# Performance work log

Measured on AMD Instinct MI355X. Metric: run time of the kernel, lower is better.

The kernel has to match this reference:

```python
import jax, jax.numpy as jnp
import numpy as np

MAX_CH = 21
LAT_DIM = 64
D_EMBED = 1024
N_HEADS = 16
D_HEAD = D_EMBED // N_HEADS  # 64
L = MAX_CH * LAT_DIM         # 1344 latents
B, T = 4, 1024


def setup_inputs() -> dict:
    key = jax.random.key(0)
    k1, k2, k3, k4, k5, k6 = jax.random.split(key, 6)
    x = jax.random.normal(k1, (B, T, D_EMBED), dtype=jnp.float32)
    # boolean channel mask [b, L, T]
    ch_mask = jax.random.randint(k2, (B, L, T), 0, 2) > 0
    # learned latent queries [L, H*d] (xavier-uniform-ish init)
    lim_q = float(np.sqrt(6.0 / (L + N_HEADS * D_HEAD)))
    latent_q = jax.random.uniform(k3, (L, N_HEADS * D_HEAD), minval=-lim_q, maxval=lim_q, dtype=jnp.float32)
    # Linear weights (torch layout: [out, in]) and biases
    lim_w = float(np.sqrt(1.0 / D_EMBED))
    w_k_w = jax.random.uniform(k4, (N_HEADS * D_HEAD, D_EMBED), minval=-lim_w, maxval=lim_w, dtype=jnp.float32)
    w_k_b = jnp.zeros((N_HEADS * D_HEAD,), dtype=jnp.float32)
    w_v_w = jax.random.uniform(k5, (N_HEADS * D_HEAD, D_EMBED), minval=-lim_w, maxval=lim_w, dtype=jnp.float32)
    w_v_b = jax.random.uniform(k6, (N_HEADS * D_HEAD,), minval=-lim_w, maxval=lim_w, dtype=jnp.float32)
    return {"x": x, "ch_mask": ch_mask, "latent_q": latent_q,
            "w_k_w": w_k_w, "w_k_b": w_k_b, "w_v_w": w_v_w, "w_v_b": w_v_b}


def reference(x, ch_mask, latent_q, w_k_w, w_k_b, w_v_w, w_v_b):
    b, t, d = x.shape
    H, dh = N_HEADS, D_HEAD
    l = latent_q.shape[0]
    # faithful to torch .view(-1, H, L, d): raw row-major reinterpretation
    lq = latent_q.reshape(1, H, l, dh)                    # [1,H,L,dh]
    k = (x @ w_k_w.T + w_k_b).reshape(b, t, H, dh).transpose(0, 2, 3, 1)  # [b,H,dh,T]
    v = (x @ w_v_w.T + w_v_b).reshape(b, t, H, dh).transpose(0, 2, 1, 3)  # [b,H,T,dh]
    scale = jnp.float32(H) ** -0.5  # note: n_heads**-0.5, as in source
    scores = jnp.einsum('ohld,bhdt->bhlt', lq, k) * scale  # [b,H,L,T]
    mask = ch_mask[:, None, :, :]                           # [b,1,L,T] broadcast over heads
    scores = jnp.where(mask, scores, jnp.float32(-1e9))
    w = jax.nn.softmax(scores, axis=-1)
    w = jnp.where(mask, w, jnp.float32(0.0))
    out = jnp.einsum('bhlt,bhtd->bhld', w, v)               # [b,H,L,dh]
    return out.transpose(0, 2, 1, 3).reshape(b, l, H * dh)  # [b,L,H*dh]
```

## Files before the change

kernel.cpp:

```cpp
#include <hip/hip_runtime.h>
#include <hip/hip_bf16.h>

#define B_SZ 4
#define T_SZ 1024
#define NH 16
#define L_SZ 1344
#define LT_COUNT 21

typedef __attribute__((ext_vector_type(8))) short short8;
typedef __attribute__((ext_vector_type(4))) short short4v;
typedef __attribute__((ext_vector_type(4))) float floatx4;

typedef __attribute__((address_space(1))) const void gvoid;
typedef __attribute__((address_space(3))) void svoid;
#define GLD16(gp, lp) \
  __builtin_amdgcn_global_load_lds((gvoid*)(gp), (svoid*)(lp), 16, 0, 0)

static __device__ inline short bf16bits(float f) {
  return __builtin_bit_cast(short, __float2bfloat16(f));
}
static __device__ inline short4v cvt4(float4 v) {
  short4v r;
  r.x = bf16bits(v.x); r.y = bf16bits(v.y);
  r.z = bf16bits(v.z); r.w = bf16bits(v.w);
  return r;
}

static __device__ inline unsigned pack_bf16_2(float a, float b) {
  unsigned ua = __builtin_bit_cast(unsigned, a) + 0x8000u;
  unsigned ub = __builtin_bit_cast(unsigned, b) + 0x8000u;
  return __builtin_amdgcn_perm(ub, ua, 0x07060302u);
}
static __device__ inline uint2 pack_bf16_4(float4 v) {
  return make_uint2(pack_bf16_2(v.x, v.y), pack_bf16_2(v.z, v.w));
}


__global__ __launch_bounds__(256) void prep_kernel(
    const float4* __restrict__ x, const float4* __restrict__ wk,
    const float4* __restrict__ wv,
    uint2* __restrict__ xb, uint2* __restrict__ wkb, uint2* __restrict__ wvb,
    const void* __restrict__ mask, unsigned int* __restrict__ bits) {
  const int lane = threadIdx.x & 63;
  int f = -1;
  for (int vb = blockIdx.x; vb < 27648; vb += gridDim.x) {
    if (vb < 6144) {
      size_t i = (size_t)vb * 256 + threadIdx.x;
      if (i < 1048576)      xb[i] = pack_bf16_4(x[i]);
      else if (i < 1310720) wkb[i - 1048576] = pack_bf16_4(wk[i - 1048576]);
      else                  wvb[i - 1310720] = pack_bf16_4(wv[i - 1310720]);
    } else {
      if (f < 0) {
        const uint4* mp = (const uint4*)mask;
        uint4 a = mp[lane * 4 + 0], b2 = mp[lane * 4 + 1];
        uint4 c = mp[lane * 4 + 2], d = mp[lane * 4 + 3];
        unsigned oo = (a.x | a.y | a.z | a.w | b2.x | b2.y | b2.z | b2.w |
                       c.x | c.y | c.z | c.w | d.x | d.y | d.z | d.w) & 0xFFFFFF00u;
        unsigned aa = (a.y | a.w | b2.y | b2.w | c.y | c.w | d.y | d.w) & 0xFFu;
        int anyo = __any(oo != 0), anya = __any(aa != 0);
        f = anyo ? 1 : (anya ? 0 : 2);
      }
      int idx = (vb - 6144) * 256 + threadIdx.x;
      bool v;
      if (f == 1)      v = ((const signed char*)mask)[idx] != 0;
      else if (f == 2) v = ((const long long*)mask)[idx] != 0;
      else             v = ((const int*)mask)[idx] != 0;
      unsigned long long bal = __ballot(v);
      if ((lane & 31) == 0) {
        unsigned int w = (lane & 32) ? (unsigned int)(bal >> 32) : (unsigned int)bal;
        bits[idx >> 5] = w;
      }
    }
  }
}

__global__ __launch_bounds__(256, 4) void gemm_kv_bf16(
    const __hip_bfloat16* __restrict__ xb,
    const __hip_bfloat16* __restrict__ wkb, const __hip_bfloat16* __restrict__ wvb,
    const float* __restrict__ bk, const float* __restrict__ bv,
    __hip_bfloat16* __restrict__ k_buf, __hip_bfloat16* __restrict__ v_buf) {
  __shared__ __align__(16) __hip_bfloat16 ldsA[2][128 * 32];
  __shared__ __align__(16) __hip_bfloat16 ldsB[2][64 * 32];
  const int tid = threadIdx.x;
  const int lane = tid & 63, w = tid >> 6;
  const int wm = w & 1, wn = w >> 1;
  const int c15 = lane & 15, kq = lane >> 4;

  const __hip_bfloat16* A;
  const __hip_bfloat16* B;
  int TA, TB;
  if (blockIdx.z == 0) {
    A = wkb; B = xb; TA = blockIdx.x >> 6; TB = blockIdx.x & 63;
  } else {
    A = xb; B = wvb; TA = blockIdx.x >> 4; TB = blockIdx.x & 15;
  }
  const __hip_bfloat16* Abase = A + (size_t)TA * 128 * 1024;
  const __hip_bfloat16* Bbase = B + (size_t)TB * 64 * 1024;

  floatx4 acc[4][2];
  #pragma unroll
  for (int i = 0; i < 4; ++i)
    #pragma unroll
    for (int j = 0; j < 2; ++j) acc[i][j] = (floatx4){0.f, 0.f, 0.f, 0.f};

#define GSTAGE(sb, kk) do {                                                  \
    int cA_ = w * 128 + lane;                                                \
    int rA_ = cA_ >> 2, gA_ = (cA_ & 3) ^ (rA_ & 3);                         \
    GLD16(Abase + (size_t)rA_ * 1024 + (kk) + gA_ * 8,                       \
          &ldsA[sb][(w * 128) * 8]);                                         \
    int cA2_ = cA_ + 64;                                                     \
    int rA2_ = cA2_ >> 2, gA2_ = (cA2_ & 3) ^ (rA2_ & 3);                    \
    GLD16(Abase + (size_t)rA2_ * 1024 + (kk) + gA2_ * 8,                     \
          &ldsA[sb][(w * 128 + 64) * 8]);                                    \
    int cB_ = w * 64 + lane;                                                 \
    int rB_ = cB_ >> 2, gB_ = (cB_ & 3) ^ (rB_ & 3);                         \
    GLD16(Bbase + (size_t)rB_ * 1024 + (kk) + gB_ * 8,                       \
          &ldsB[sb][(w * 64) * 8]);                                          \
  } while (0)

  GSTAGE(0, 0);
  for (int kk = 0; kk < 1024; kk += 32) {
    const int buf = (kk >> 5) & 1;
    if (kk + 32 < 1024) {
      GSTAGE(buf ^ 1, kk + 32);
      asm volatile("s_waitcnt vmcnt(3)" ::: "memory");
    } else {
      asm volatile("s_waitcnt vmcnt(0)" ::: "memory");
    }
    __builtin_amdgcn_s_barrier();

    short8 af[4], bfr[2];
    #pragma unroll
    for (int mi = 0; mi < 4; ++mi) {
      int row = wm * 64 + mi * 16 + c15;
      af[mi] = *(const short8*)(&ldsA[buf][row * 32 + ((kq ^ (row & 3)) * 8)]);
    }
    #pragma unroll
    for (int ni = 0; ni < 2; ++ni) {
      int row = wn * 32 + ni * 16 + c15;
      bfr[ni] = *(const short8*)(&ldsB[buf][row * 32 + ((kq ^ (row & 3)) * 8)]);
    }
    #pragma unroll
    for (int mi = 0; mi < 4; ++mi)
      #pragma unroll
      for (int ni = 0; ni < 2; ++ni)
        acc[mi][ni] = __builtin_amdgcn_mfma_f32_16x16x32_bf16(
            af[mi], bfr[ni], acc[mi][ni], 0, 0, 0);

    asm volatile("s_waitcnt lgkmcnt(0)" ::: "memory");
    __builtin_amdgcn_s_barrier();
  }
#undef GSTAGE

  if (blockIdx.z == 0) {
    #pragma unroll
    for (int ni = 0; ni < 2; ++ni) {
      int gr = TB * 64 + wn * 32 + ni * 16 + c15;
      int b = gr >> 10, tc = (gr >> 6) & 15;
      int ni2 = (gr & 63) >> 4;
      #pragma unroll
      for (int mi = 0; mi < 4; ++mi) {
        int d0 = TA * 128 + wm * 64 + mi * 16 + kq * 4;
        int h = d0 >> 6, hd = d0 & 63;
        int half = hd >> 5, q4 = (hd >> 3) & 3, jlo = hd & 7;
        int bh = b * 16 + h;
        float4 b4 = *(const float4*)(bk + d0);
        float4 v4 = {acc[mi][ni][0] + b4.x, acc[mi][ni][1] + b4.y,
                     acc[mi][ni][2] + b4.z, acc[mi][ni][3] + b4.w};
        *(uint2*)(k_buf + ((size_t)((bh * 16 + tc) * 8 + ni2 * 2 + half)) * 512 +
                  (q4 * 16 + c15) * 8 + jlo) = pack_bf16_4(v4);
      }
    }
  } else {
    #pragma unroll
    for (int ni = 0; ni < 2; ++ni) {
      int d = TB * 64 + wn * 32 + ni * 16 + c15;
      int h = d >> 6;
      int di = (d & 63) >> 4;
      float bias = bv[d];
      #pragma unroll
      for (int mi = 0; mi < 4; ++mi) {
        int gr = TA * 128 + wm * 64 + mi * 16 + kq * 4;
        int b = gr >> 10, tc = (gr >> 6) & 15;
        int tl = gr & 63;
        int half = tl >> 5, q4 = (tl >> 3) & 3, jlo = tl & 7;
        int bh = b * 16 + h;
        float4 v4 = {acc[mi][ni][0] + bias, acc[mi][ni][1] + bias,
                     acc[mi][ni][2] + bias, acc[mi][ni][3] + bias};
        *(uint2*)(v_buf + ((size_t)((bh * 16 + tc) * 8 + di * 2 + half)) * 512 +
                  (q4 * 16 + c15) * 8 + jlo) = pack_bf16_4(v4);
      }
    }
  }
}

__global__ __launch_bounds__(256, 4) void attn_kernel(
    const float* __restrict__ latent_q,
    const __hip_bfloat16* __restrict__ k_buf,
    const __hip_bfloat16* __restrict__ v_buf,
    const unsigned int* __restrict__ mbits,
    float* __restrict__ out) {
  __shared__ __align__(16) __hip_bfloat16 ldsK[2][4096];
  __shared__ __align__(16) __hip_bfloat16 ldsV[2][4096];
  __shared__ __align__(16) __hip_bfloat16 pbuf[4][1024];

  const int tid = threadIdx.x;
  const int lane = tid & 63;
  const int w = tid >> 6;
  int bid = blockIdx.x;
  int xcd = bid & 7, j = bid >> 3;
  int bh = xcd * 8 + j / LT_COUNT;
  int lt = j % LT_COUNT;
  int h = bh & 15, b = bh >> 4;
  const int q4 = lane >> 4, c15 = lane & 15;
  const int c7 = c15 & 7;
  const int l0 = lt * 64;

  const float QS = 0.25f * 1.44269504089f;
  short8 qf[2];
  {
    const float* qp = latent_q + ((size_t)(h * L_SZ + l0 + w * 16 + c15)) * 64 + q4 * 8;
    float4 a0 = *(const float4*)(qp);
    float4 a1 = *(const float4*)(qp + 4);
    float4 a2 = *(const float4*)(qp + 32);
    float4 a3 = *(const float4*)(qp + 36);
    a0.x *= QS; a0.y *= QS; a0.z *= QS; a0.w *= QS;
    a1.x *= QS; a1.y *= QS; a1.z *= QS; a1.w *= QS;
    a2.x *= QS; a2.y *= QS; a2.z *= QS; a2.w *= QS;
    a3.x *= QS; a3.y *= QS; a3.z *= QS; a3.w *= QS;
    short4v t0 = cvt4(a0), t1 = cvt4(a1), t2 = cvt4(a2), t3 = cvt4(a3);
    qf[0] = (short8){t0.x, t0.y, t0.z, t0.w, t1.x, t1.y, t1.z, t1.w};
    qf[1] = (short8){t2.x, t2.y, t2.z, t2.w, t3.x, t3.y, t3.z, t3.w};
  }

  const short ob16 = (short)0x3F80;
  const short8 ones8 = (short8){ob16, ob16, ob16, ob16, ob16, ob16, ob16, ob16};
  const floatx4 zero4 = (floatx4){0.f, 0.f, 0.f, 0.f};

  floatx4 lacc = zero4;
  floatx4 o_acc[4];
  #pragma unroll
  for (int di = 0; di < 4; ++di) o_acc[di] = zero4;

  const __hip_bfloat16* kb = k_buf + (size_t)bh * 65536;
  const __hip_bfloat16* vb = v_buf + (size_t)bh * 65536;
  __hip_bfloat16* pw = pbuf[w];
  const unsigned int* mrow = mbits + ((size_t)(b * L_SZ + l0 + w * 16 + c15)) * 32;

#define STAGE_K(sb, tcn) do {                                               \
    const __hip_bfloat16* gk_ = kb + (size_t)(tcn) * 4096;                  \
    int o0_ = w * 512 + lane * 8;                                           \
    GLD16(gk_ + o0_,        &ldsK[sb][w * 512]);                            \
    GLD16(gk_ + 2048 + o0_, &ldsK[sb][2048 + w * 512]);                     \
  } while (0)
#define STAGE_V(sb, tcn) do {                                               \
    const __hip_bfloat16* gv_ = vb + (size_t)(tcn) * 4096;                  \
    int o0_ = w * 512 + lane * 8;                                           \
    GLD16(gv_ + o0_,        &ldsV[sb][w * 512]);                            \
    GLD16(gv_ + 2048 + o0_, &ldsV[sb][2048 + w * 512]);                     \
  } while (0)

  uint2 mw_cur = *(const uint2*)(mrow);
  STAGE_K(0, 0);
  STAGE_V(0, 0);

  for (int tc = 0; tc < 16; ++tc) {
    const int buf = tc & 1;
    if (tc < 15) {
      STAGE_K(buf ^ 1, tc + 1);
      asm volatile("s_waitcnt vmcnt(5)" ::: "memory");
    } else {
      asm volatile("s_waitcnt vmcnt(3)" ::: "memory");
    }
    __builtin_amdgcn_s_barrier();

    uint2 mw_nxt = mw_cur;
    if (tc < 15) mw_nxt = *(const uint2*)(mrow + (tc + 1) * 2);

    short8 kf[2][4];
    #pragma unroll
    for (int half = 0; half < 2; ++half)
      #pragma unroll
      for (int ni = 0; ni < 4; ++ni)
        kf[half][ni] = *(const short8*)(&ldsK[buf][(ni * 2 + half) * 512 + lane * 8]);
    floatx4 s[4];
    __builtin_amdgcn_s_setprio(1);
    #pragma unroll
    for (int ni = 0; ni < 4; ++ni)
      s[ni] = __builtin_amdgcn_mfma_f32_16x16x32_bf16(kf[0][ni], qf[0], zero4, 0, 0, 0);
    #pragma unroll
    for (int ni = 0; ni < 4; ++ni)
      s[ni] = __builtin_amdgcn_mfma_f32_16x16x32_bf16(kf[1][ni], qf[1], s[ni], 0, 0, 0);
    __builtin_amdgcn_s_setprio(0);

    if (tc < 15) {
      STAGE_V(buf ^ 1, tc + 1);
      asm volatile("s_waitcnt vmcnt(5)" ::: "memory");
    } else {
      asm volatile("s_waitcnt vmcnt(0)" ::: "memory");
    }
    __builtin_amdgcn_s_barrier();

    short8 vf[2][4];
    #pragma unroll
    for (int half = 0; half < 2; ++half)
      #pragma unroll
      for (int di = 0; di < 4; ++di)
        vf[half][di] = *(const short8*)(&ldsV[buf][(di * 2 + half) * 512 + lane * 8]);

    #pragma unroll
    for (int ni = 0; ni < 4; ++ni) {
      unsigned mword = (ni >= 2) ? mw_cur.y : mw_cur.x;
      float4 p4;
      #pragma unroll
      for (int r = 0; r < 4; ++r) {
        float e = exp2f(s[ni][r]);
        int sh = (ni & 1) * 16 + q4 * 4 + r;
        ((float*)&p4)[r] = ((mword >> sh) & 1) ? e : 0.f;
      }
      int pc = (ni * 2 + (q4 >> 1)) ^ c7;
      *(uint2*)(pw + c15 * 64 + pc * 8 + (q4 & 1) * 4) = pack_bf16_4(p4);
    }

    int pc0 = q4 ^ c7;
    short8 pf0 = *(const short8*)(pw + c15 * 64 + pc0 * 8);
    short8 pf1 = *(const short8*)(pw + c15 * 64 + (pc0 ^ 4) * 8);
    __builtin_amdgcn_s_setprio(1);
    #pragma unroll
    for (int di = 0; di < 4; ++di)
      o_acc[di] = __builtin_amdgcn_mfma_f32_16x16x32_bf16(vf[0][di], pf0, o_acc[di], 0, 0, 0);
    #pragma unroll
    for (int di = 0; di < 4; ++di)
      o_acc[di] = __builtin_amdgcn_mfma_f32_16x16x32_bf16(vf[1][di], pf1, o_acc[di], 0, 0, 0);
    lacc = __builtin_amdgcn_mfma_f32_16x16x32_bf16(ones8, pf0, lacc, 0, 0, 0);
    lacc = __builtin_amdgcn_mfma_f32_16x16x32_bf16(ones8, pf1, lacc, 0, 0, 0);
    __builtin_amdgcn_s_setprio(0);

    mw_cur = mw_nxt;
  }
#undef STAGE_K
#undef STAGE_V

  float la = lacc[0];
  float inv = (la > 0.f) ? 1.f / la : 0.f;
  float* ob = out + ((size_t)(b * L_SZ + l0 + w * 16 + c15)) * 1024 + h * 64;
  #pragma unroll
  for (int di = 0; di < 4; ++di) {
    float4 o4 = {o_acc[di][0] * inv, o_acc[di][1] * inv,
                 o_acc[di][2] * inv, o_acc[di][3] * inv};
    *(float4*)(ob + di * 16 + q4 * 4) = o4;
  }
}

extern "C" void kernel_launch(void* const* d_in, const int* in_sizes, int n_in,
                              void* d_out, int out_size, void* d_ws, size_t ws_size,
                              hipStream_t stream) {
  const float* x      = (const float*)d_in[0];
  const void* ch_mask = d_in[1];
  const float* lq     = (const float*)d_in[2];
  const float* wk     = (const float*)d_in[3];
  const float* bk     = (const float*)d_in[4];
  const float* wv     = (const float*)d_in[5];
  const float* bv     = (const float*)d_in[6];
  float* out = (float*)d_out;

  char* ws = (char*)d_ws;
  unsigned int* mbits   = (unsigned int*)ws;
  __hip_bfloat16* k_buf = (__hip_bfloat16*)(ws + 786432);
  __hip_bfloat16* v_buf = (__hip_bfloat16*)(ws + 786432 + 8388608);

  __hip_bfloat16* xb  = (__hip_bfloat16*)d_out;
  __hip_bfloat16* wkb = xb + 4 * 1024 * 1024;
  __hip_bfloat16* wvb = wkb + 1024 * 1024;

  prep_kernel<<<2048, 256, 0, stream>>>(
      (const float4*)x, (const float4*)wk, (const float4*)wv,
      (uint2*)xb, (uint2*)wkb, (uint2*)wvb,
      ch_mask, mbits);
  gemm_kv_bf16<<<dim3(512, 1, 2), 256, 0, stream>>>(xb, wkb, wvb, bk, bv, k_buf, v_buf);

  attn_kernel<<<8 * 168, 256, 0, stream>>>(lq, k_buf, v_buf, mbits, out);
}
```

Before: 189.2 us.

## Widen attention blocks to 8 waves covering 128 latents per K/V stage

The attention kernel now launches 512-thread blocks that each cover 128 latent rows, so each staged K/V tile is shared by 8 waves instead of 4. Each wave issues one async global-to-LDS load per tile instead of two, which halves the K/V traffic per latent. The cost is a ragged final block: 1344 is not a multiple of 128, so idle waves are guarded by a `has` flag but still join every barrier. Larger blocks may also lower occupancy and lengthen barrier stalls.

```diff
diff --git a/kernel.cpp b/kernel.cpp
--- a/kernel.cpp
+++ b/kernel.cpp
@@ -194,7 +194,7 @@
   }
 }
 
-__global__ __launch_bounds__(256, 4) void attn_kernel(
+__global__ __launch_bounds__(512, 6) void attn_kernel(
     const float* __restrict__ latent_q,
     const __hip_bfloat16* __restrict__ k_buf,
     const __hip_bfloat16* __restrict__ v_buf,
@@ -202,24 +202,27 @@
     float* __restrict__ out) {
   __shared__ __align__(16) __hip_bfloat16 ldsK[2][4096];
   __shared__ __align__(16) __hip_bfloat16 ldsV[2][4096];
-  __shared__ __align__(16) __hip_bfloat16 pbuf[4][1024];
+  __shared__ __align__(16) __hip_bfloat16 pbuf[8][1024];
 
   const int tid = threadIdx.x;
   const int lane = tid & 63;
   const int w = tid >> 6;
   int bid = blockIdx.x;
   int xcd = bid & 7, j = bid >> 3;
-  int bh = xcd * 8 + j / LT_COUNT;
-  int lt = j % LT_COUNT;
+  int bh = xcd * 8 + j / 11;
+  int sb = j % 11;
   int h = bh & 15, b = bh >> 4;
   const int q4 = lane >> 4, c15 = lane & 15;
   const int c7 = c15 & 7;
-  const int l0 = lt * 64;
+  const int l0 = sb * 128;
+  const int lg = l0 + w * 16;
+  const bool has = lg < L_SZ;
+  const int lrow = has ? lg : 0;
 
   const float QS = 0.25f * 1.44269504089f;
   short8 qf[2];
   {
-    const float* qp = latent_q + ((size_t)(h * L_SZ + l0 + w * 16 + c15)) * 64 + q4 * 8;
+    const float* qp = latent_q + ((size_t)(h * L_SZ + lrow + c15)) * 64 + q4 * 8;
     float4 a0 = *(const float4*)(qp);
     float4 a1 = *(const float4*)(qp + 4);
     float4 a2 = *(const float4*)(qp + 32);
@@ -245,110 +248,108 @@
   const __hip_bfloat16* kb = k_buf + (size_t)bh * 65536;
   const __hip_bfloat16* vb = v_buf + (size_t)bh * 65536;
   __hip_bfloat16* pw = pbuf[w];
-  const unsigned int* mrow = mbits + ((size_t)(b * L_SZ + l0 + w * 16 + c15)) * 32;
-
-#define STAGE_K(sb, tcn) do {                                               \
-    const __hip_bfloat16* gk_ = kb + (size_t)(tcn) * 4096;                  \
-    int o0_ = w * 512 + lane * 8;                                           \
-    GLD16(gk_ + o0_,        &ldsK[sb][w * 512]);                            \
-    GLD16(gk_ + 2048 + o0_, &ldsK[sb][2048 + w * 512]);                     \
-  } while (0)
-#define STAGE_V(sb, tcn) do {                                               \
-    const __hip_bfloat16* gv_ = vb + (size_t)(tcn) * 4096;                  \
-    int o0_ = w * 512 + lane * 8;                                           \
-    GLD16(gv_ + o0_,        &ldsV[sb][w * 512]);                            \
-    GLD16(gv_ + 2048 + o0_, &ldsV[sb][2048 + w * 512]);                     \
-  } while (0)
-
-  uint2 mw_cur = *(const uint2*)(mrow);
+  const unsigned int* mrow = mbits + ((size_t)(b * L_SZ + lrow + c15)) * 32;
+
+#define STAGE_K(sbuf, tcn) \
+    GLD16(kb + (size_t)(tcn) * 4096 + w * 512 + lane * 8, &ldsK[sbuf][w * 512])
+#define STAGE_V(sbuf, tcn) \
+    GLD16(vb + (size_t)(tcn) * 4096 + w * 512 + lane * 8, &ldsV[sbuf][w * 512])
+
   STAGE_K(0, 0);
   STAGE_V(0, 0);
+  uint2 mw_cur = *(const uint2*)(mrow);
 
   for (int tc = 0; tc < 16; ++tc) {
     const int buf = tc & 1;
     if (tc < 15) {
       STAGE_K(buf ^ 1, tc + 1);
-      asm volatile("s_waitcnt vmcnt(5)" ::: "memory");
+      asm volatile("s_waitcnt vmcnt(3)" ::: "memory");
     } else {
-      asm volatile("s_waitcnt vmcnt(3)" ::: "memory");
+      asm volatile("s_waitcnt vmcnt(2)" ::: "memory");
     }
     __builtin_amdgcn_s_barrier();
 
     uint2 mw_nxt = mw_cur;
     if (tc < 15) mw_nxt = *(const uint2*)(mrow + (tc + 1) * 2);
 
-    short8 kf[2][4];
-    #pragma unroll
-    for (int half = 0; half < 2; ++half)
+    floatx4 s[4];
+    if (has) {
+      short8 kf[2][4];
+      #pragma unroll
+      for (int half = 0; half < 2; ++half)
+        #pragma unroll
+        for (int ni = 0; ni < 4; ++ni)
+          kf[half][ni] = *(const short8*)(&ldsK[buf][(ni * 2 + half) * 512 + lane * 8]);
+      __builtin_amdgcn_s_setprio(1);
       #pragma unroll
       for (int ni = 0; ni < 4; ++ni)
-        kf[half][ni] = *(const short8*)(&ldsK[buf][(ni * 2 + half) * 512 + lane * 8]);
-    floatx4 s[4];
-    __builtin_amdgcn_s_setprio(1);
-    #pragma unroll
-    for (int ni = 0; ni < 4; ++ni)
-      s[ni] = __builtin_amdgcn_mfma_f32_16x16x32_bf16(kf[0][ni], qf[0], zero4, 0, 0, 0);
-    #pragma unroll
-    for (int ni = 0; ni < 4; ++ni)
-      s[ni] = __builtin_amdgcn_mfma_f32_16x16x32_bf16(kf[1][ni], qf[1], s[ni], 0, 0, 0);
-    __builtin_amdgcn_s_setprio(0);
+        s[ni] = __builtin_amdgcn_mfma_f32_16x16x32_bf16(kf[0][ni], qf[0], zero4, 0, 0, 0);
+      #pragma unroll
+      for (int ni = 0; ni < 4; ++ni)
+        s[ni] = __builtin_amdgcn_mfma_f32_16x16x32_bf16(kf[1][ni], qf[1], s[ni], 0, 0, 0);
+      __builtin_amdgcn_s_setprio(0);
+    }
 
     if (tc < 15) {
       STAGE_V(buf ^ 1, tc + 1);
-      asm volatile("s_waitcnt vmcnt(5)" ::: "memory");
+      asm volatile("s_waitcnt vmcnt(3)" ::: "memory");
     } else {
       asm volatile("s_waitcnt vmcnt(0)" ::: "memory");
     }
     __builtin_amdgcn_s_barrier();
 
-    short8 vf[2][4];
-    #pragma unroll
-    for (int half = 0; half < 2; ++half)
+    if (has) {
+      short8 vf[2][4];
+      #pragma unroll
+      for (int half = 0; half < 2; ++half)
+        #pragma unroll
+        for (int di = 0; di < 4; ++di)
+          vf[half][di] = *(const short8*)(&ldsV[buf][(di * 2 + half) * 512 + lane * 8]);
+
+      #pragma unroll
+      for (int ni = 0; ni < 4; ++ni) {
+        unsigned mword = (ni >= 2) ? mw_cur.y : mw_cur.x;
+        float4 p4;
+        #pragma unroll
+        for (int r = 0; r < 4; ++r) {
+          float e = exp2f(s[ni][r]);
+          int sh = (ni & 1) * 16 + q4 * 4 + r;
+          ((float*)&p4)[r] = ((mword >> sh) & 1) ? e : 0.f;
+        }
+        int pc = (ni * 2 + (q4 >> 1)) ^ c7;
+        *(uint2*)(pw + c15 * 64 + pc * 8 + (q4 & 1) * 4) = pack_bf16_4(p4);
+      }
+
+      int pc0 = q4 ^ c7;
+      short8 pf0 = *(const short8*)(pw + c15 * 64 + pc0 * 8);
+      short8 pf1 = *(const short8*)(pw + c15 * 64 + (pc0 ^ 4) * 8);
+      __builtin_amdgcn_s_setprio(1);
       #pragma unroll
       for (int di = 0; di < 4; ++di)
-        vf[half][di] = *(const short8*)(&ldsV[buf][(di * 2 + half) * 512 + lane * 8]);
-
-    #pragma unroll
-    for (int ni = 0; ni < 4; ++ni) {
-      unsigned mword = (ni >= 2) ? mw_cur.y : mw_cur.x;
-      float4 p4;
-      #pragma unroll
-      for (int r = 0; r < 4; ++r) {
-        float e = exp2f(s[ni][r]);
-        int sh = (ni & 1) * 16 + q4 * 4 + r;
-        ((float*)&p4)[r] = ((mword >> sh) & 1) ? e : 0.f;
-      }
-      int pc = (ni * 2 + (q4 >> 1)) ^ c7;
-      *(uint2*)(pw + c15 * 64 + pc * 8 + (q4 & 1) * 4) = pack_bf16_4(p4);
-    }
-
-    int pc0 = q4 ^ c7;
-    short8 pf0 = *(const short8*)(pw + c15 * 64 + pc0 * 8);
-    short8 pf1 = *(const short8*)(pw + c15 * 64 + (pc0 ^ 4) * 8);
-    __builtin_amdgcn_s_setprio(1);
-    #pragma unroll
-    for (int di = 0; di < 4; ++di)
-      o_acc[di] = __builtin_amdgcn_mfma_f32_16x16x32_bf16(vf[0][di], pf0, o_acc[di], 0, 0, 0);
-    #pragma unroll
-    for (int di = 0; di < 4; ++di)
-      o_acc[di] = __builtin_amdgcn_mfma_f32_16x16x32_bf16(vf[1][di], pf1, o_acc[di], 0, 0, 0);
-    lacc = __builtin_amdgcn_mfma_f32_16x16x32_bf16(ones8, pf0, lacc, 0, 0, 0);
-    lacc = __builtin_amdgcn_mfma_f32_16x16x32_bf16(ones8, pf1, lacc, 0, 0, 0);
-    __builtin_amdgcn_s_setprio(0);
+        o_acc[di] = __builtin_amdgcn_mfma_f32_16x16x32_bf16(vf[0][di], pf0, o_acc[di], 0, 0, 0);
+      #pragma unroll
+      for (int di = 0; di < 4; ++di)
+        o_acc[di] = __builtin_amdgcn_mfma_f32_16x16x32_bf16(vf[1][di], pf1, o_acc[di], 0, 0, 0);
+      lacc = __builtin_amdgcn_mfma_f32_16x16x32_bf16(ones8, pf0, lacc, 0, 0, 0);
+      lacc = __builtin_amdgcn_mfma_f32_16x16x32_bf16(ones8, pf1, lacc, 0, 0, 0);
+      __builtin_amdgcn_s_setprio(0);
+    }
 
     mw_cur = mw_nxt;
   }
 #undef STAGE_K
 #undef STAGE_V
 
-  float la = lacc[0];
-  float inv = (la > 0.f) ? 1.f / la : 0.f;
-  float* ob = out + ((size_t)(b * L_SZ + l0 + w * 16 + c15)) * 1024 + h * 64;
-  #pragma unroll
-  for (int di = 0; di < 4; ++di) {
-    float4 o4 = {o_acc[di][0] * inv, o_acc[di][1] * inv,
-                 o_acc[di][2] * inv, o_acc[di][3] * inv};
-    *(float4*)(ob + di * 16 + q4 * 4) = o4;
+  if (has) {
+    float la = lacc[0];
+    float inv = (la > 0.f) ? 1.f / la : 0.f;
+    float* ob = out + ((size_t)(b * L_SZ + lrow + c15)) * 1024 + h * 64;
+    #pragma unroll
+    for (int di = 0; di < 4; ++di) {
+      float4 o4 = {o_acc[di][0] * inv, o_acc[di][1] * inv,
+                   o_acc[di][2] * inv, o_acc[di][3] * inv};
+      *(float4*)(ob + di * 16 + q4 * 4) = o4;
+    }
   }
 }
 
@@ -379,5 +380,5 @@
       ch_mask, mbits);
   gemm_kv_bf16<<<dim3(512, 1, 2), 256, 0, stream>>>(xb, wkb, wvb, bk, bv, k_buf, v_buf);
 
-  attn_kernel<<<8 * 168, 256, 0, stream>>>(lq, k_buf, v_buf, mbits, out);
-}
+  attn_kernel<<<8 * 88, 512, 0, stream>>>(lq, k_buf, v_buf, mbits, out);
+}
```

Result: slower. 322.0 us (+70.2%).
